# Performance work log

Hardware: AMD Instinct MI355X
Metric: run time of the kernel (lower is better)

The kernel has to match this reference:

```python
import jax, jax.numpy as jnp
import numpy as np

B, T, E, H = 32, 2048, 512, 512


def setup_inputs() -> dict:
    key = jax.random.key(0)
    k1, k2, k3 = jax.random.split(key, 3)
    scale_w = 1.0 / np.sqrt(E)
    scale_u = 1.0 / np.sqrt(H)
    return {
        "src_seq": jax.random.normal(k1, (B, T, E), dtype=jnp.float32),
        "W": jax.random.normal(k2, (E, 4 * H), dtype=jnp.float32) * scale_w,
        "U": jax.random.normal(k3, (H, 4 * H), dtype=jnp.float32) * scale_u,
        "b": jnp.zeros((4 * H,), dtype=jnp.float32),
        "h0": jnp.zeros((B, H), dtype=jnp.float32),
        "c0": jnp.zeros((B, H), dtype=jnp.float32),
    }


def reference(src_seq, W, U, b, h0, c0):
    """LSTM encoder: scan an LSTMCell over time.

    Returns (output, encoding_hidden_states [T,B,H], final_state), where
    output == final hidden state, matching the original forward().
    """

    def step(carry, x_t):
        h, c = carry
        # Fused gate pre-activations: [B, 4H], keras LSTMCell order i,f,g,o
        z = x_t @ W + h @ U + b
        i, f, g, o = jnp.split(z, 4, axis=-1)
        i = jax.nn.sigmoid(i)
        f = jax.nn.sigmoid(f)
        g = jnp.tanh(g)
        o = jax.nn.sigmoid(o)
        c_new = f * c + i * g
        h_new = o * jnp.tanh(c_new)
        return (h_new, c_new), h_new

    xs = jnp.swapaxes(src_seq, 0, 1)  # [T, B, E]
    (h_T, c_T), hs = jax.lax.scan(step, (h0, c0), xs)
    # (output, list-of-per-step hidden states stacked, final hidden state)
    return h_T, hs, h_T
```

## Files before the change

### kernel.cpp

```cpp
#include <hip/hip_runtime.h>
#include <stdint.h>

#define T_STEPS 2048
#define BATCH 32
#define EDIM 512
#define HDIM 512

typedef __attribute__((ext_vector_type(8))) short bf16x8;
typedef __attribute__((ext_vector_type(4))) float f32x4;
typedef unsigned long long u64t;

#define FIXED_WS 0x831000ull

__device__ inline unsigned short f2bf(float x){
    unsigned u = __float_as_uint(x);
    unsigned r = (u + 0x7fffu + ((u >> 16) & 1u)) >> 16;
    return (unsigned short)r;
}
__device__ inline float bf2f(unsigned short s){
    return __uint_as_float(((unsigned)s) << 16);
}

__global__ void prep_kernel(const float* __restrict__ W, const float* __restrict__ U,
                            const float* __restrict__ h0,
                            unsigned short* __restrict__ Wh, unsigned short* __restrict__ Wl,
                            unsigned short* __restrict__ Uh, unsigned short* __restrict__ Ul,
                            unsigned* __restrict__ hbuf){
    int idx = blockIdx.x * blockDim.x + threadIdx.x;
    int stride = gridDim.x * blockDim.x;
    const int total = 2 * EDIM * 2048;
    for (int i = idx; i < total; i += stride){
        int mat = i >> 20;
        int r = i & 1048575;
        int k = r >> 11;
        int col = r & 2047;
        float v = (mat ? U : W)[(size_t)k * 2048 + col];
        unsigned short hi = f2bf(v);
        unsigned short lo = f2bf(v - bf2f(hi));
        int cg = (col & 511) >> 4;
        int hc = col & 15;
        int g  = col >> 9;
        int kb = k >> 5;
        int kgrp = (k >> 3) & 3;
        int j = k & 7;
        size_t dst = (size_t)cg * 32768 + (size_t)kb * 2048 + (size_t)g * 512
                   + (size_t)(kgrp * 16 + hc) * 8 + j;
        if (mat){ Uh[dst] = hi; Ul[dst] = lo; } else { Wh[dst] = hi; Wl[dst] = lo; }
    }
    for (int i = idx; i < BATCH * HDIM; i += stride){
        float v = h0[i];
        unsigned short hi = f2bf(v);
        unsigned short lo = f2bf(v - bf2f(hi));
        hbuf[i] = (unsigned)hi | ((unsigned)lo << 16);
    }
}

__global__ __launch_bounds__(256) void xw_gemm_chunk(
        const float* __restrict__ src,
        const unsigned short* __restrict__ Wh, const unsigned short* __restrict__ Wl,
        float* __restrict__ xWc, int t0){
    const int bid = blockIdx.x;
    const int mtile = bid >> 5;
    const int cg = bid & 31;
    const int tid = threadIdx.x;
    const int lane = tid & 63;
    const int w = tid >> 6;
    const int tc = mtile * 4 + w;
    const int t = t0 + tc;
    const int lc = lane & 15;
    const int kgrp = lane >> 4;

    const uint4* WhF = reinterpret_cast<const uint4*>(Wh) + (size_t)cg * 4096;
    const uint4* WlF = reinterpret_cast<const uint4*>(Wl) + (size_t)cg * 4096;

    f32x4 acc[2][4];
    #pragma unroll
    for (int bt = 0; bt < 2; bt++)
        #pragma unroll
        for (int ct = 0; ct < 4; ct++)
            #pragma unroll
            for (int r = 0; r < 4; r++) acc[bt][ct][r] = 0.f;

    for (int kb = 0; kb < 16; kb++){
        bf16x8 ah[2], al[2];
        #pragma unroll
        for (int bt = 0; bt < 2; bt++){
            const float* xp = src + ((size_t)(bt * 16 + lc) * 2048 + t) * 512 + kb * 32 + kgrp * 8;
            float xv[8];
            *reinterpret_cast<float4*>(&xv[0]) = *reinterpret_cast<const float4*>(xp);
            *reinterpret_cast<float4*>(&xv[4]) = *reinterpret_cast<const float4*>(xp + 4);
            #pragma unroll
            for (int j = 0; j < 8; j++){
                unsigned short hi = f2bf(xv[j]);
                ah[bt][j] = (short)hi;
                al[bt][j] = (short)f2bf(xv[j] - bf2f(hi));
            }
        }
        #pragma unroll
        for (int ct = 0; ct < 4; ct++){
            uint4 bh4 = WhF[kb * 256 + ct * 64 + lane];
            uint4 bl4 = WlF[kb * 256 + ct * 64 + lane];
            bf16x8 bh = *reinterpret_cast<bf16x8*>(&bh4);
            bf16x8 bl = *reinterpret_cast<bf16x8*>(&bl4);
            #pragma unroll
            for (int bt = 0; bt < 2; bt++){
                acc[bt][ct] = __builtin_amdgcn_mfma_f32_16x16x32_bf16(ah[bt], bh, acc[bt][ct], 0, 0, 0);
                acc[bt][ct] = __builtin_amdgcn_mfma_f32_16x16x32_bf16(ah[bt], bl, acc[bt][ct], 0, 0, 0);
                acc[bt][ct] = __builtin_amdgcn_mfma_f32_16x16x32_bf16(al[bt], bh, acc[bt][ct], 0, 0, 0);
            }
        }
    }
    #pragma unroll
    for (int bt = 0; bt < 2; bt++)
        #pragma unroll
        for (int ct = 0; ct < 4; ct++)
            #pragma unroll
            for (int r = 0; r < 4; r++){
                int row_b = bt * 16 + kgrp * 4 + r;
                xWc[((size_t)tc * 32 + row_b) * 2048 + ct * 512 + cg * 16 + lc] = acc[bt][ct][r];
            }
}

__global__ __launch_bounds__(512, 1) void lstm_scan_fast(
        const float* __restrict__ bias, const float* __restrict__ c0,
        const unsigned short* __restrict__ Uh, const unsigned short* __restrict__ Ul,
        unsigned* __restrict__ hbuf, unsigned* __restrict__ cnt,
        const float* __restrict__ xWc, float* __restrict__ c_ws,
        float* __restrict__ out, int t0, int tlen){
    const int tid  = threadIdx.x;
    const int cg   = blockIdx.x;
    const int lane = tid & 63;
    const int w    = tid >> 6;
    const int bt   = w >> 2;
    const int kq   = w & 3;
    const int lc   = lane & 15;
    const int kgrp = lane >> 4;
    const int row  = bt * 16 + lc;

    __shared__ float z_lds[4][BATCH][65];

    const int cb  = tid >> 4;
    const int chc = tid & 15;
    const int col = cg * 16 + chc;
    float c_state = (t0 == 0) ? c0[(size_t)cb * HDIM + col] : c_ws[(size_t)cb * HDIM + col];
    float bias_g[4];
    #pragma unroll
    for (int g = 0; g < 4; g++) bias_g[g] = bias[g * HDIM + col];

    const uint4* UhF = reinterpret_cast<const uint4*>(Uh) + (size_t)cg * 4096;
    const uint4* UlF = reinterpret_cast<const uint4*>(Ul) + (size_t)cg * 4096;
    bf16x8 ufh[4][4], ufl[4][4];
    #pragma unroll
    for (int i = 0; i < 4; i++){
        int kb = kq * 4 + i;
        #pragma unroll
        for (int ct = 0; ct < 4; ct++){
            uint4 a  = UhF[kb * 256 + ct * 64 + lane];
            uint4 b2 = UlF[kb * 256 + ct * 64 + lane];
            ufh[i][ct] = *reinterpret_cast<bf16x8*>(&a);
            ufl[i][ct] = *reinterpret_cast<bf16x8*>(&b2);
        }
    }

    f32x4 acc[4];
    #pragma unroll
    for (int ct = 0; ct < 4; ct++)
        #pragma unroll
        for (int r = 0; r < 4; r++) acc[ct][r] = 0.f;

    for (int t = t0; t < t0 + tlen; t++){
        const float* xwp = xWc + ((size_t)(t - t0) * 32 + cb) * 2048 + col;
        float zx0 = xwp[0], zx1 = xwp[512], zx2 = xwp[1024], zx3 = xwp[1536];

        if (t > 0){
            if (w == 0){
                const unsigned need = 32u * (unsigned)((t + 1) >> 1);
                while (__hip_atomic_load(&cnt[t & 1], __ATOMIC_RELAXED, __HIP_MEMORY_SCOPE_AGENT) < need)
                    __builtin_amdgcn_s_sleep(1);
            }
            __syncthreads();
        }

        const u64t* hp = reinterpret_cast<const u64t*>(hbuf)
                       + (size_t)(t & 1) * 8192 + (size_t)row * 256;
        u64t hv[16];
        #pragma unroll
        for (int i = 0; i < 4; i++){
            int base = (kq * 4 + i) * 16 + kgrp * 4;
            #pragma unroll
            for (int jp = 0; jp < 4; jp++)
                hv[i * 4 + jp] = __hip_atomic_load(hp + base + jp,
                                                   __ATOMIC_RELAXED, __HIP_MEMORY_SCOPE_AGENT);
        }

        #pragma unroll
        for (int i = 0; i < 4; i++){
            bf16x8 ah, al;
            #pragma unroll
            for (int jp = 0; jp < 4; jp++){
                u64t q = hv[i * 4 + jp];
                unsigned a = (unsigned)q;
                unsigned b = (unsigned)(q >> 32);
                ah[jp * 2    ] = (short)(a & 0xffffu); al[jp * 2    ] = (short)(a >> 16);
                ah[jp * 2 + 1] = (short)(b & 0xffffu); al[jp * 2 + 1] = (short)(b >> 16);
            }
            #pragma unroll
            for (int ct = 0; ct < 4; ct++){
                acc[ct] = __builtin_amdgcn_mfma_f32_16x16x32_bf16(ah, ufh[i][ct], acc[ct], 0, 0, 0);
                acc[ct] = __builtin_amdgcn_mfma_f32_16x16x32_bf16(ah, ufl[i][ct], acc[ct], 0, 0, 0);
                acc[ct] = __builtin_amdgcn_mfma_f32_16x16x32_bf16(al, ufh[i][ct], acc[ct], 0, 0, 0);
            }
        }

        #pragma unroll
        for (int ct = 0; ct < 4; ct++)
            #pragma unroll
            for (int r = 0; r < 4; r++)
                z_lds[kq][bt * 16 + kgrp * 4 + r][ct * 16 + lc] = acc[ct][r];
        __syncthreads();

        {
            float z0 = z_lds[0][cb][chc]      + z_lds[1][cb][chc]      + z_lds[2][cb][chc]      + z_lds[3][cb][chc]      + zx0 + bias_g[0];
            float z1 = z_lds[0][cb][16 + chc] + z_lds[1][cb][16 + chc] + z_lds[2][cb][16 + chc] + z_lds[3][cb][16 + chc] + zx1 + bias_g[1];
            float z2 = z_lds[0][cb][32 + chc] + z_lds[1][cb][32 + chc] + z_lds[2][cb][32 + chc] + z_lds[3][cb][32 + chc] + zx2 + bias_g[2];
            float z3 = z_lds[0][cb][48 + chc] + z_lds[1][cb][48 + chc] + z_lds[2][cb][48 + chc] + z_lds[3][cb][48 + chc] + zx3 + bias_g[3];
            float ig = 1.f / (1.f + __expf(-z0));
            float fg = 1.f / (1.f + __expf(-z1));
            float gg = tanhf(z2);
            float og = 1.f / (1.f + __expf(-z3));
            float cn = fg * c_state + ig * gg;
            c_state = cn;
            float hn = og * tanhf(cn);
            out[16384 + ((size_t)t * BATCH + cb) * HDIM + col] = hn;
            if (t == T_STEPS - 1){
                out[(size_t)cb * HDIM + col] = hn;
                out[16384 + (size_t)T_STEPS * BATCH * HDIM + (size_t)cb * HDIM + col] = hn;
            }
            unsigned short hi = f2bf(hn);
            unsigned short lo = f2bf(hn - bf2f(hi));
            __hip_atomic_store(&hbuf[(size_t)((t + 1) & 1) * (BATCH * HDIM) + (size_t)cb * HDIM + col],
                               (unsigned)hi | ((unsigned)lo << 16),
                               __ATOMIC_RELAXED, __HIP_MEMORY_SCOPE_AGENT);
        }
        __syncthreads();
        if (tid == 0)
            __hip_atomic_fetch_add(&cnt[(t + 1) & 1], 1u,
                                   __ATOMIC_RELAXED, __HIP_MEMORY_SCOPE_AGENT);

        #pragma unroll
        for (int ct = 0; ct < 4; ct++)
            #pragma unroll
            for (int r = 0; r < 4; r++) acc[ct][r] = 0.f;
    }
    c_ws[(size_t)cb * HDIM + col] = c_state;
}

__global__ __launch_bounds__(512, 2) void lstm_scan_r7(
        const float* __restrict__ src, const float* __restrict__ bias,
        const float* __restrict__ c0,
        const unsigned short* __restrict__ Wh, const unsigned short* __restrict__ Wl,
        const unsigned short* __restrict__ Uh, const unsigned short* __restrict__ Ul,
        unsigned* __restrict__ hbuf, unsigned* __restrict__ cnt,
        float* __restrict__ out){
    const int tid  = threadIdx.x;
    const int cg   = blockIdx.x;
    const int lane = tid & 63;
    const int w    = tid >> 6;
    const int bt   = w >> 2;
    const int kq   = w & 3;
    const int lc   = lane & 15;
    const int kgrp = lane >> 4;
    const int row  = bt * 16 + lc;

    __shared__ float z_lds[4][BATCH][65];

    const int cb  = tid >> 4;
    const int chc = tid & 15;
    const int col = cg * 16 + chc;
    float c_state = c0[(size_t)cb * HDIM + col];
    float bias_g[4];
    #pragma unroll
    for (int g = 0; g < 4; g++) bias_g[g] = bias[g * HDIM + col];

    const uint4* WhF = reinterpret_cast<const uint4*>(Wh) + (size_t)cg * 4096;
    const uint4* WlF = reinterpret_cast<const uint4*>(Wl) + (size_t)cg * 4096;
    const uint4* UhF = reinterpret_cast<const uint4*>(Uh) + (size_t)cg * 4096;
    const uint4* UlF = reinterpret_cast<const uint4*>(Ul) + (size_t)cg * 4096;

    f32x4 acc[4];
    #pragma unroll
    for (int ct = 0; ct < 4; ct++)
        #pragma unroll
        for (int r = 0; r < 4; r++) acc[ct][r] = 0.f;

    auto phaseA = [&](int t){
        #pragma unroll
        for (int i = 0; i < 4; i++){
            int kb = kq * 4 + i;
            const float* xp = src + ((size_t)row * T_STEPS + t) * EDIM + kb * 32 + kgrp * 8;
            float xv[8];
            *reinterpret_cast<float4*>(&xv[0]) = *reinterpret_cast<const float4*>(xp);
            *reinterpret_cast<float4*>(&xv[4]) = *reinterpret_cast<const float4*>(xp + 4);
            bf16x8 ah, al;
            #pragma unroll
            for (int j = 0; j < 8; j++){
                unsigned short hi = f2bf(xv[j]);
                ah[j] = (short)hi;
                al[j] = (short)f2bf(xv[j] - bf2f(hi));
            }
            #pragma unroll
            for (int ct = 0; ct < 4; ct++){
                uint4 bh4 = WhF[kb * 256 + ct * 64 + lane];
                uint4 bl4 = WlF[kb * 256 + ct * 64 + lane];
                bf16x8 bh = *reinterpret_cast<bf16x8*>(&bh4);
                bf16x8 bl = *reinterpret_cast<bf16x8*>(&bl4);
                acc[ct] = __builtin_amdgcn_mfma_f32_16x16x32_bf16(ah, bh, acc[ct], 0, 0, 0);
                acc[ct] = __builtin_amdgcn_mfma_f32_16x16x32_bf16(ah, bl, acc[ct], 0, 0, 0);
                acc[ct] = __builtin_amdgcn_mfma_f32_16x16x32_bf16(al, bh, acc[ct], 0, 0, 0);
            }
        }
    };

    phaseA(0);

    for (int t = 0; t < T_STEPS; t++){
        if (t > 0){
            if (w == 0){
                const unsigned need = 32u * (unsigned)((t + 1) >> 1);
                while (__hip_atomic_load(&cnt[t & 1], __ATOMIC_RELAXED, __HIP_MEMORY_SCOPE_AGENT) < need)
                    __builtin_amdgcn_s_sleep(1);
            }
            __syncthreads();
        }

        const u64t* hp = reinterpret_cast<const u64t*>(hbuf)
                       + (size_t)(t & 1) * 8192 + (size_t)row * 256;
        u64t hv[16];
        #pragma unroll
        for (int i = 0; i < 4; i++){
            int base = (kq * 4 + i) * 16 + kgrp * 4;
            #pragma unroll
            for (int jp = 0; jp < 4; jp++)
                hv[i * 4 + jp] = __hip_atomic_load(hp + base + jp,
                                                   __ATOMIC_RELAXED, __HIP_MEMORY_SCOPE_AGENT);
        }

        #pragma unroll
        for (int i = 0; i < 4; i++){
            int kb = kq * 4 + i;
            bf16x8 ah, al;
            #pragma unroll
            for (int jp = 0; jp < 4; jp++){
                u64t q = hv[i * 4 + jp];
                unsigned a = (unsigned)q;
                unsigned b = (unsigned)(q >> 32);
                ah[jp * 2    ] = (short)(a & 0xffffu); al[jp * 2    ] = (short)(a >> 16);
                ah[jp * 2 + 1] = (short)(b & 0xffffu); al[jp * 2 + 1] = (short)(b >> 16);
            }
            #pragma unroll
            for (int ct = 0; ct < 4; ct++){
                uint4 uh4 = UhF[kb * 256 + ct * 64 + lane];
                uint4 ul4 = UlF[kb * 256 + ct * 64 + lane];
                bf16x8 uh = *reinterpret_cast<bf16x8*>(&uh4);
                bf16x8 ul = *reinterpret_cast<bf16x8*>(&ul4);
                acc[ct] = __builtin_amdgcn_mfma_f32_16x16x32_bf16(ah, uh, acc[ct], 0, 0, 0);
                acc[ct] = __builtin_amdgcn_mfma_f32_16x16x32_bf16(ah, ul, acc[ct], 0, 0, 0);
                acc[ct] = __builtin_amdgcn_mfma_f32_16x16x32_bf16(al, uh, acc[ct], 0, 0, 0);
            }
        }

        #pragma unroll
        for (int ct = 0; ct < 4; ct++)
            #pragma unroll
            for (int r = 0; r < 4; r++)
                z_lds[kq][bt * 16 + kgrp * 4 + r][ct * 16 + lc] = acc[ct][r];
        __syncthreads();

        {
            float z[4];
            #pragma unroll
            for (int g = 0; g < 4; g++)
                z[g] = z_lds[0][cb][g * 16 + chc] + z_lds[1][cb][g * 16 + chc]
                     + z_lds[2][cb][g * 16 + chc] + z_lds[3][cb][g * 16 + chc] + bias_g[g];
            float ig = 1.f / (1.f + __expf(-z[0]));
            float fg = 1.f / (1.f + __expf(-z[1]));
            float gg = tanhf(z[2]);
            float og = 1.f / (1.f + __expf(-z[3]));
            float cn = fg * c_state + ig * gg;
            c_state = cn;
            float hn = og * tanhf(cn);
            out[16384 + ((size_t)t * BATCH + cb) * HDIM + col] = hn;
            if (t == T_STEPS - 1){
                out[(size_t)cb * HDIM + col] = hn;
                out[16384 + (size_t)T_STEPS * BATCH * HDIM + (size_t)cb * HDIM + col] = hn;
            }
            unsigned short hi = f2bf(hn);
            unsigned short lo = f2bf(hn - bf2f(hi));
            __hip_atomic_store(&hbuf[(size_t)((t + 1) & 1) * (BATCH * HDIM) + (size_t)cb * HDIM + col],
                               (unsigned)hi | ((unsigned)lo << 16),
                               __ATOMIC_RELAXED, __HIP_MEMORY_SCOPE_AGENT);
        }
        __syncthreads();
        if (tid == 0)
            __hip_atomic_fetch_add(&cnt[(t + 1) & 1], 1u,
                                   __ATOMIC_RELAXED, __HIP_MEMORY_SCOPE_AGENT);

        #pragma unroll
        for (int ct = 0; ct < 4; ct++)
            #pragma unroll
            for (int r = 0; r < 4; r++) acc[ct][r] = 0.f;
        if (t + 1 < T_STEPS) phaseA(t + 1);
    }
}

extern "C" void kernel_launch(void* const* d_in, const int* in_sizes, int n_in,
                              void* d_out, int out_size, void* d_ws, size_t ws_size,
                              hipStream_t stream){
    const float* src = (const float*)d_in[0];
    const float* W   = (const float*)d_in[1];
    const float* U   = (const float*)d_in[2];
    const float* b   = (const float*)d_in[3];
    const float* h0  = (const float*)d_in[4];
    const float* c0  = (const float*)d_in[5];
    float* out = (float*)d_out;
    char* ws = (char*)d_ws;

    int TCH = 0;
    const int cand[5] = {256, 128, 64, 32, 16};
    for (int i = 0; i < 5; i++){
        if (FIXED_WS + (size_t)cand[i] * 262144ull <= ws_size){ TCH = cand[i]; break; }
    }

    if (TCH > 0){
        unsigned*       hbuf = (unsigned*)(ws);
        unsigned*       cnt  = (unsigned*)(ws + 0x020000ull);
        float*          c_ws = (float*)(ws + 0x021000ull);
        unsigned short* Wh   = (unsigned short*)(ws + 0x031000ull);
        unsigned short* Wl   = (unsigned short*)(ws + 0x231000ull);
        unsigned short* Uh   = (unsigned short*)(ws + 0x431000ull);
        unsigned short* Ul   = (unsigned short*)(ws + 0x631000ull);
        float*          xWc  = (float*)(ws + FIXED_WS);

        hipMemsetAsync(cnt, 0, 8, stream);
        prep_kernel<<<1024, 256, 0, stream>>>(W, U, h0, Wh, Wl, Uh, Ul, hbuf);
        const int nch = T_STEPS / TCH;
        for (int i = 0; i < nch; i++){
            int t0 = i * TCH;
            xw_gemm_chunk<<<(TCH / 4) * 32, 256, 0, stream>>>(src, Wh, Wl, xWc, t0);
            lstm_scan_fast<<<32, 512, 0, stream>>>(b, c0, Uh, Ul, hbuf, cnt,
                                                   xWc, c_ws, out, t0, TCH);
        }
    } else {
        unsigned*       hbuf = (unsigned*)(ws);
        unsigned*       cnt  = (unsigned*)(ws + 0x20000);
        unsigned short* Wh   = (unsigned short*)(ws + 0x21000);
        unsigned short* Wl   = Wh + 1048576;
        unsigned short* Uh   = Wl + 1048576;
        unsigned short* Ul   = Uh + 1048576;
        hipMemsetAsync(cnt, 0, 8, stream);
        prep_kernel<<<1024, 256, 0, stream>>>(W, U, h0, Wh, Wl, Uh, Ul, hbuf);
        lstm_scan_r7<<<32, 512, 0, stream>>>(src, b, c0, Wh, Wl, Uh, Ul, hbuf, cnt, out);
    }
}
```

Measured before the change: 12.10 ms.

## Replace counter barrier with per-block step flags, move output stores after signal

The shared atomic counter barrier is replaced by per-block monotonically increasing step flags. Every wave now polls all 32 flags with a wave vote, which removes the wave-0 spin followed by __syncthreads. Output stores are moved after the flag store so they leave the critical path between timesteps. Gate activations switch to fast reciprocal and exp-based tanh, trading some accuracy at the extremes for fewer instructions. All waves polling raises memory traffic during the wait.

```diff
diff --git a/kernel.cpp b/kernel.cpp
--- a/kernel.cpp
+++ b/kernel.cpp
@@ -19,6 +19,14 @@
 }
 __device__ inline float bf2f(unsigned short s){
     return __uint_as_float(((unsigned)s) << 16);
+}
+__device__ inline float sigmoid_f(float x){
+    return __builtin_amdgcn_rcpf(1.f + __expf(-x));
+}
+__device__ inline float tanh_f(float x){
+    float xc = fminf(30.f, fmaxf(-30.f, x));
+    float e = __expf(2.f * xc);
+    return (e - 1.f) * __builtin_amdgcn_rcpf(e + 1.f);
 }
 
 __global__ void prep_kernel(const float* __restrict__ W, const float* __restrict__ U,
@@ -124,7 +132,7 @@
 __global__ __launch_bounds__(512, 1) void lstm_scan_fast(
         const float* __restrict__ bias, const float* __restrict__ c0,
         const unsigned short* __restrict__ Uh, const unsigned short* __restrict__ Ul,
-        unsigned* __restrict__ hbuf, unsigned* __restrict__ cnt,
+        unsigned* __restrict__ hbuf, unsigned* __restrict__ done,
         const float* __restrict__ xWc, float* __restrict__ c_ws,
         float* __restrict__ out, int t0, int tlen){
     const int tid  = threadIdx.x;
@@ -173,12 +181,13 @@
         float zx0 = xwp[0], zx1 = xwp[512], zx2 = xwp[1024], zx3 = xwp[1536];
 
         if (t > 0){
-            if (w == 0){
-                const unsigned need = 32u * (unsigned)((t + 1) >> 1);
-                while (__hip_atomic_load(&cnt[t & 1], __ATOMIC_RELAXED, __HIP_MEMORY_SCOPE_AGENT) < need)
-                    __builtin_amdgcn_s_sleep(1);
-            }
-            __syncthreads();
+            const unsigned tgt = (unsigned)t;
+            while (true){
+                unsigned f = __hip_atomic_load(&done[lane & 31],
+                                               __ATOMIC_RELAXED, __HIP_MEMORY_SCOPE_AGENT);
+                if (__all(f >= tgt)) break;
+                __builtin_amdgcn_s_sleep(1);
+            }
         }
 
         const u64t* hp = reinterpret_cast<const u64t*>(hbuf)
@@ -219,23 +228,19 @@
                 z_lds[kq][bt * 16 + kgrp * 4 + r][ct * 16 + lc] = acc[ct][r];
         __syncthreads();
 
+        float hn;
         {
             float z0 = z_lds[0][cb][chc]      + z_lds[1][cb][chc]      + z_lds[2][cb][chc]      + z_lds[3][cb][chc]      + zx0 + bias_g[0];
             float z1 = z_lds[0][cb][16 + chc] + z_lds[1][cb][16 + chc] + z_lds[2][cb][16 + chc] + z_lds[3][cb][16 + chc] + zx1 + bias_g[1];
             float z2 = z_lds[0][cb][32 + chc] + z_lds[1][cb][32 + chc] + z_lds[2][cb][32 + chc] + z_lds[3][cb][32 + chc] + zx2 + bias_g[2];
             float z3 = z_lds[0][cb][48 + chc] + z_lds[1][cb][48 + chc] + z_lds[2][cb][48 + chc] + z_lds[3][cb][48 + chc] + zx3 + bias_g[3];
-            float ig = 1.f / (1.f + __expf(-z0));
-            float fg = 1.f / (1.f + __expf(-z1));
-            float gg = tanhf(z2);
-            float og = 1.f / (1.f + __expf(-z3));
+            float ig = sigmoid_f(z0);
+            float fg = sigmoid_f(z1);
+            float gg = tanh_f(z2);
+            float og = sigmoid_f(z3);
             float cn = fg * c_state + ig * gg;
             c_state = cn;
-            float hn = og * tanhf(cn);
-            out[16384 + ((size_t)t * BATCH + cb) * HDIM + col] = hn;
-            if (t == T_STEPS - 1){
-                out[(size_t)cb * HDIM + col] = hn;
-                out[16384 + (size_t)T_STEPS * BATCH * HDIM + (size_t)cb * HDIM + col] = hn;
-            }
+            hn = og * tanh_f(cn);
             unsigned short hi = f2bf(hn);
             unsigned short lo = f2bf(hn - bf2f(hi));
             __hip_atomic_store(&hbuf[(size_t)((t + 1) & 1) * (BATCH * HDIM) + (size_t)cb * HDIM + col],
@@ -244,8 +249,14 @@
         }
         __syncthreads();
         if (tid == 0)
-            __hip_atomic_fetch_add(&cnt[(t + 1) & 1], 1u,
-                                   __ATOMIC_RELAXED, __HIP_MEMORY_SCOPE_AGENT);
+            __hip_atomic_store(&done[cg], (unsigned)(t + 1),
+                               __ATOMIC_RELAXED, __HIP_MEMORY_SCOPE_AGENT);
+
+        out[16384 + ((size_t)t * BATCH + cb) * HDIM + col] = hn;
+        if (t == T_STEPS - 1){
+            out[(size_t)cb * HDIM + col] = hn;
+            out[16384 + (size_t)T_STEPS * BATCH * HDIM + (size_t)cb * HDIM + col] = hn;
+        }
 
         #pragma unroll
         for (int ct = 0; ct < 4; ct++)
@@ -433,7 +444,7 @@
 
     if (TCH > 0){
         unsigned*       hbuf = (unsigned*)(ws);
-        unsigned*       cnt  = (unsigned*)(ws + 0x020000ull);
+        unsigned*       done = (unsigned*)(ws + 0x020000ull);
         float*          c_ws = (float*)(ws + 0x021000ull);
         unsigned short* Wh   = (unsigned short*)(ws + 0x031000ull);
         unsigned short* Wl   = (unsigned short*)(ws + 0x231000ull);
@@ -441,13 +452,13 @@
         unsigned short* Ul   = (unsigned short*)(ws + 0x631000ull);
         float*          xWc  = (float*)(ws + FIXED_WS);
 
-        hipMemsetAsync(cnt, 0, 8, stream);
+        hipMemsetAsync(done, 0, 128, stream);
         prep_kernel<<<1024, 256, 0, stream>>>(W, U, h0, Wh, Wl, Uh, Ul, hbuf);
         const int nch = T_STEPS / TCH;
         for (int i = 0; i < nch; i++){
             int t0 = i * TCH;
             xw_gemm_chunk<<<(TCH / 4) * 32, 256, 0, stream>>>(src, Wh, Wl, xWc, t0);
-            lstm_scan_fast<<<32, 512, 0, stream>>>(b, c0, Uh, Ul, hbuf, cnt,
+            lstm_scan_fast<<<32, 512, 0, stream>>>(b, c0, Uh, Ul, hbuf, done,
                                                    xWc, c_ws, out, t0, TCH);
         }
     } else {
```

Result: faster. 11.71 ms (median of 2 runs) (-3.3%).
